# Kernel optimization log

Hardware: AMD Instinct MI355X
Metric: run time of the kernel (lower is better)

Reference implementation:

```python
import jax, jax.numpy as jnp
import numpy as np
from jax import lax

REPLACE_PROB = 0.12
B, I, T = 16, 256, 8192


def setup_inputs() -> dict:
    key = jax.random.key(0)
    p = REPLACE_PROB
    s = 1.0 - 2.0 * p
    # probs[p2, p1, :] = P(x_t | x_{t-2}=p2, x_{t-1}=p1); all rows [p, s, p]
    # except [2,1] which disallows jitter value 0 (the '012' triplet) and renormalizes.
    probs = np.tile(np.array([p, s, p], dtype=np.float32), (3, 3, 1))
    probs[2, 1, :] = np.array([0.0, s / (p + s), p / (p + s)], dtype=np.float32)
    x = jax.random.normal(jax.random.fold_in(key, 1), (B, I, T), dtype=jnp.float32)
    return {"x": x, "probs": jnp.asarray(probs)}


def _gen_mindex(key, probs, n_batch, n_time):
    """Sample the (n_batch, n_time+1) jitter code sequence in alphabet {0,1,2}.
    mindex[:, 0:2] = 1, mindex[:, n_time] = 1, interior sampled by a
    2nd-order Markov scan: P(x_t | x_{t-2}, x_{t-1}) = probs[p2, p1]."""
    log_probs = jnp.log(probs)  # -inf for the zeroed entry is fine for categorical

    def one_seq(k):
        ks = jax.random.split(k, n_time - 2)

        def step(carry, kk):
            p2, p1 = carry
            j = jax.random.categorical(kk, log_probs[p2, p1]).astype(jnp.int32)
            return (p1, j), j

        _, js = lax.scan(step, (jnp.int32(1), jnp.int32(1)), ks)
        return js  # (n_time - 2,)

    js = jax.vmap(one_seq)(jax.random.split(key, n_batch))  # (B, T-2)
    ones2 = jnp.ones((n_batch, 2), jnp.int32)
    ones1 = jnp.ones((n_batch, 1), jnp.int32)
    return jnp.concatenate([ones2, js, ones1], axis=1)  # (B, T+1)


def reference(x, probs):
    n_batch, n_chan, n_time = x.shape
    mindex = _gen_mindex(jax.random.key(42), probs, n_batch, n_time)
    # torch code: mindex += (arange(T+1) - 2); y[b] = index_select(x[b], 1, mindex[b, 1:])
    # => source index for output position t is (t) + (jitter - 1), jitter in {0,1,2}
    idx = mindex[:, 1:] + (jnp.arange(n_time, dtype=jnp.int32) - 1)  # (B, T), in [0, T-1]
    return jnp.take_along_axis(x, idx[:, None, :], axis=2)  # (B, I, T)
```

## Files before the change

kernel.cpp:

```cpp
#include <hip/hip_runtime.h>
#include <stdint.h>

#define T_LEN 8192
#define NSTEP 8190
#define NB 16
#define NCH 256

__device__ __forceinline__ uint32_t rotl32(uint32_t v, int r) {
  return (v << r) | (v >> (32 - r));
}

__device__ __forceinline__ void tf2x32(uint32_t k0, uint32_t k1, uint32_t x0, uint32_t x1,
                                       uint32_t& o0, uint32_t& o1) {
  uint32_t ks2 = k0 ^ k1 ^ 0x1BD11BDAu;
  x0 += k0; x1 += k1;
#define RR(r) { x0 += x1; x1 = rotl32(x1, (r)); x1 ^= x0; }
  RR(13) RR(15) RR(26) RR(6)   x0 += k1;  x1 += ks2 + 1u;
  RR(17) RR(29) RR(16) RR(24)  x0 += ks2; x1 += k0 + 2u;
  RR(13) RR(15) RR(26) RR(6)   x0 += k0;  x1 += k1 + 3u;
  RR(17) RR(29) RR(16) RR(24)  x0 += k1;  x1 += ks2 + 4u;
  RR(13) RR(15) RR(26) RR(6)   x0 += ks2; x1 += k0 + 5u;
#undef RR
  o0 = x0; o1 = x1;
}

__global__ __launch_bounds__(256) void k_decide(const float* __restrict__ probs,
                                                uint8_t* __restrict__ dec) {
  int j = blockIdx.x * 256 + threadIdx.x;
  int b = blockIdx.y;
  if (j >= NSTEP) return;

  uint32_t kb0, kb1;
  tf2x32(0u, 42u, 0u, (uint32_t)b, kb0, kb1);

  uint32_t s0, s1;
  tf2x32(kb0, kb1, 0u, (uint32_t)j, s0, s1);

  uint32_t bits[3];
  {
    uint32_t y0, y1;
    tf2x32(s0, s1, 0u, 0u, y0, y1); bits[0] = y0 ^ y1;
    tf2x32(s0, s1, 0u, 1u, y0, y1); bits[1] = y0 ^ y1;
    tf2x32(s0, s1, 0u, 2u, y0, y1); bits[2] = y0 ^ y1;
  }

  double g[3];
#pragma unroll
  for (int c = 0; c < 3; ++c) {
    uint32_t k = bits[c] >> 9;
    float u = k ? (float)k * 0x1p-23f : 1.17549435e-38f;
    g[c] = -log(-log((double)u));
  }

  double lp = log((double)probs[0]);
  double ls = log((double)probs[1]);
  double l1 = log((double)probs[2 * 9 + 1 * 3 + 1]);
  double l2 = log((double)probs[2 * 9 + 1 * 3 + 2]);

  double v0 = lp + g[0], v1 = ls + g[1], v2 = lp + g[2];
  int n = 0; double best = v0;
  if (v1 > best) { n = 1; best = v1; }
  if (v2 > best) { n = 2; }
  int sp = (l1 + g[1] >= l2 + g[2]) ? 1 : 2;

  dec[b * NSTEP + j] = (uint8_t)(n | (sp << 2));
}

__device__ __forceinline__ uint64_t compose_map(uint64_t f, uint64_t g) {
  uint64_t r = 0;
#pragma unroll
  for (int st = 0; st < 9; ++st) {
    uint32_t fs = (uint32_t)((f >> (4 * st)) & 15u);
    uint32_t gs = (uint32_t)((g >> (4 * fs)) & 15u);
    r |= ((uint64_t)gs) << (4 * st);
  }
  return r;
}

__device__ __forceinline__ uint64_t shflup64(uint64_t v, int delta) {
  int lo = __shfl_up((int)(uint32_t)v, delta, 64);
  int hi = __shfl_up((int)(uint32_t)(v >> 32), delta, 64);
  return (((uint64_t)(uint32_t)hi) << 32) | (uint32_t)lo;
}

#define IDENT_MAP 0x876543210ull

__global__ __launch_bounds__(256) void k_scan(const uint8_t* __restrict__ dec,
                                              int* __restrict__ idxbuf) {
  int b = blockIdx.x;
  int tid = threadIdx.x;
  int lane = tid & 63, wave = tid >> 6;
  int begin = tid * 32;
  const uint8_t* row = dec + b * NSTEP;

  uint64_t M = IDENT_MAP;
#pragma unroll
  for (int t = 0; t < 32; ++t) {
    int step = begin + t;
    if (step < NSTEP) {
      int d = row[step];
      uint32_t n = d & 3u, s = (d >> 2) & 3u;
      uint64_t Mn = 0;
#pragma unroll
      for (int st = 0; st < 9; ++st) {
        uint32_t u = (uint32_t)((M >> (4 * st)) & 15u);
        uint32_t div3 = (u * 11u) >> 5;
        uint32_t p1 = u - 3u * div3;
        uint32_t jj = (u == 7u) ? s : n;
        Mn |= ((uint64_t)(p1 * 3u + jj)) << (4 * st);
      }
      M = Mn;
    }
  }

  uint64_t I = M;
#pragma unroll
  for (int off = 1; off < 64; off <<= 1) {
    uint64_t Mp = shflup64(I, off);
    uint64_t c = compose_map(Mp, I);
    I = (lane >= off) ? c : I;
  }

  __shared__ uint64_t wmap[4];
  if (lane == 63) wmap[wave] = I;
  __syncthreads();

  uint64_t W = IDENT_MAP;
  for (int w = 0; w < wave; ++w) W = compose_map(W, wmap[w]);
  uint64_t E = shflup64(I, 1);
  if (lane == 0) E = IDENT_MAP;
  uint64_t X = compose_map(W, E);

  int state = (int)((X >> (4 * 4)) & 15u);

  int* orow = idxbuf + b * T_LEN;
#pragma unroll
  for (int t = 0; t < 32; ++t) {
    int step = begin + t;
    if (step < NSTEP) {
      int d = row[step];
      uint32_t n = d & 3u, s = (d >> 2) & 3u;
      uint32_t jj = (state == 7) ? s : n;
      uint32_t div3 = ((uint32_t)state * 11u) >> 5;
      uint32_t p1 = (uint32_t)state - 3u * div3;
      state = (int)(p1 * 3u + jj);
      orow[step + 1] = step + (int)jj;
    }
  }
  if (tid == 0) { orow[0] = 0; orow[T_LEN - 1] = T_LEN - 1; }
}

__global__ __launch_bounds__(256) void k_gather(const float* __restrict__ x,
                                                const int* __restrict__ idxbuf,
                                                float* __restrict__ out) {
  int b = blockIdx.z, i = blockIdx.y;
  int t0 = (blockIdx.x * 256 + threadIdx.x) * 4;
  const int4 id4 = *(const int4*)(idxbuf + b * T_LEN + t0);
  const float* __restrict__ xr = x + ((size_t)(b * NCH + i)) * T_LEN;
  float4 o;
  o.x = xr[id4.x];
  o.y = xr[id4.y];
  o.z = xr[id4.z];
  o.w = xr[id4.w];
  *(float4*)(out + ((size_t)(b * NCH + i)) * T_LEN + t0) = o;
}

extern "C" void kernel_launch(void* const* d_in, const int* in_sizes, int n_in,
                              void* d_out, int out_size, void* d_ws, size_t ws_size,
                              hipStream_t stream) {
  const float* x = (const float*)d_in[0];
  const float* probs = (const float*)d_in[1];
  float* out = (float*)d_out;

  uint8_t* dec = (uint8_t*)d_ws;
  int* idxbuf = (int*)((char*)d_ws + (131072));

  dim3 g1((NSTEP + 255) / 256, NB);
  k_decide<<<g1, 256, 0, stream>>>(probs, dec);

  k_scan<<<NB, 256, 0, stream>>>(dec, idxbuf);

  dim3 g3(T_LEN / (256 * 4), NCH, NB);
  k_gather<<<g3, 256, 0, stream>>>(x, idxbuf, out);
}
```

Measured before the change: 73.26 us.

## Store jitter as bytes and gather via contiguous loads plus wave shuffles

The scan kernel now writes a one-byte jitter code per position instead of a full int source index. The gather kernel reads a float4 window of x contiguously and takes each output from its neighbours, using wave shuffles for the edge elements and a direct load at wave boundaries. It also processes 4 channels per block so one byte-code load is shared. This replaces scattered per-element index gathers and shrinks index traffic, at the cost of fewer blocks and some select logic.

Measured after the change: 67.82 us. -7.4%, faster.

```diff
diff --git a/kernel.cpp b/kernel.cpp
--- a/kernel.cpp
+++ b/kernel.cpp
@@ -5,6 +5,7 @@
 #define NSTEP 8190
 #define NB 16
 #define NCH 256
+#define CB 4
 
 __device__ __forceinline__ uint32_t rotl32(uint32_t v, int r) {
   return (v << r) | (v >> (32 - r));
@@ -32,7 +33,6 @@
 
   uint32_t kb0, kb1;
   tf2x32(0u, 42u, 0u, (uint32_t)b, kb0, kb1);
-
   uint32_t s0, s1;
   tf2x32(kb0, kb1, 0u, (uint32_t)j, s0, s1);
 
@@ -86,7 +86,7 @@
 #define IDENT_MAP 0x876543210ull
 
 __global__ __launch_bounds__(256) void k_scan(const uint8_t* __restrict__ dec,
-                                              int* __restrict__ idxbuf) {
+                                              uint8_t* __restrict__ dbuf) {
   int b = blockIdx.x;
   int tid = threadIdx.x;
   int lane = tid & 63, wave = tid >> 6;
@@ -133,7 +133,7 @@
 
   int state = (int)((X >> (4 * 4)) & 15u);
 
-  int* orow = idxbuf + b * T_LEN;
+  uint8_t* orow = dbuf + b * T_LEN;
 #pragma unroll
   for (int t = 0; t < 32; ++t) {
     int step = begin + t;
@@ -144,25 +144,40 @@
       uint32_t div3 = ((uint32_t)state * 11u) >> 5;
       uint32_t p1 = (uint32_t)state - 3u * div3;
       state = (int)(p1 * 3u + jj);
-      orow[step + 1] = step + (int)jj;
+      orow[step + 1] = (uint8_t)jj;
     }
   }
-  if (tid == 0) { orow[0] = 0; orow[T_LEN - 1] = T_LEN - 1; }
+  if (tid == 0) { orow[0] = 1; orow[T_LEN - 1] = 1; }
 }
 
 __global__ __launch_bounds__(256) void k_gather(const float* __restrict__ x,
-                                                const int* __restrict__ idxbuf,
+                                                const uint8_t* __restrict__ dbuf,
                                                 float* __restrict__ out) {
-  int b = blockIdx.z, i = blockIdx.y;
-  int t0 = (blockIdx.x * 256 + threadIdx.x) * 4;
-  const int4 id4 = *(const int4*)(idxbuf + b * T_LEN + t0);
-  const float* __restrict__ xr = x + ((size_t)(b * NCH + i)) * T_LEN;
-  float4 o;
-  o.x = xr[id4.x];
-  o.y = xr[id4.y];
-  o.z = xr[id4.z];
-  o.w = xr[id4.w];
-  *(float4*)(out + ((size_t)(b * NCH + i)) * T_LEN + t0) = o;
+  int b = blockIdx.z;
+  int i0 = blockIdx.y * CB;
+  int tid = threadIdx.x;
+  int lane = tid & 63;
+  int t0 = (blockIdx.x * 256 + tid) * 4;
+
+  const uchar4 du = *(const uchar4*)(dbuf + b * T_LEN + t0);
+  const int d0 = du.x, d1 = du.y, d2 = du.z, d3 = du.w;
+
+#pragma unroll
+  for (int c = 0; c < CB; ++c) {
+    const float* __restrict__ xr = x + ((size_t)(b * NCH + i0 + c)) * T_LEN;
+    float4 v = *(const float4*)(xr + t0);
+    float left  = __shfl_up(v.w, 1);
+    float right = __shfl_down(v.x, 1);
+    if (lane == 0)  left  = (t0 > 0) ? xr[t0 - 1] : 0.0f;
+    if (lane == 63) right = (t0 + 4 < T_LEN) ? xr[t0 + 4] : 0.0f;
+
+    float4 o;
+    o.x = (d0 == 0) ? left : ((d0 == 1) ? v.x : v.y);
+    o.y = (d1 == 0) ? v.x  : ((d1 == 1) ? v.y : v.z);
+    o.z = (d2 == 0) ? v.y  : ((d2 == 1) ? v.z : v.w);
+    o.w = (d3 == 0) ? v.z  : ((d3 == 1) ? v.w : right);
+    *(float4*)(out + ((size_t)(b * NCH + i0 + c)) * T_LEN + t0) = o;
+  }
 }
 
 extern "C" void kernel_launch(void* const* d_in, const int* in_sizes, int n_in,
@@ -173,13 +188,13 @@
   float* out = (float*)d_out;
 
   uint8_t* dec = (uint8_t*)d_ws;
-  int* idxbuf = (int*)((char*)d_ws + (131072));
+  uint8_t* dbuf = (uint8_t*)d_ws + 131072;
 
   dim3 g1((NSTEP + 255) / 256, NB);
   k_decide<<<g1, 256, 0, stream>>>(probs, dec);
 
-  k_scan<<<NB, 256, 0, stream>>>(dec, idxbuf);
-
-  dim3 g3(T_LEN / (256 * 4), NCH, NB);
-  k_gather<<<g3, 256, 0, stream>>>(x, idxbuf, out);
-}
+  k_scan<<<NB, 256, 0, stream>>>(dec, dbuf);
+
+  dim3 g3(T_LEN / (256 * 4), NCH / CB, NB);
+  k_gather<<<g3, 256, 0, stream>>>(x, dbuf, out);
+}
```
